# Kernel tuning notes

Hardware: AMD Instinct MI355X
Metric: run time of the kernel (lower is better)

## Reference

```python
import jax, jax.numpy as jnp
import numpy as np

NUM_HEADS = 12


def setup_inputs() -> dict:
    key = jax.random.key(0)
    k0, k1, k2 = jax.random.split(key, 3)
    B, N, C = 32, 864, 768  # N = 2*t_h*t_w + s_h*s_w = 288 + 576
    x = jax.random.normal(k0, (B, N, C), dtype=jnp.float32)
    W_qkv = jax.random.normal(k1, (C, 3 * C), dtype=jnp.float32) * 0.02
    W_proj = jax.random.normal(k2, (C, C), dtype=jnp.float32) * 0.02
    b_proj = jnp.zeros((C,), dtype=jnp.float32)
    return {"x": x, "W_qkv": W_qkv, "W_proj": W_proj, "b_proj": b_proj,
            "t_h": 12, "t_w": 12, "s_h": 24, "s_w": 24}


def reference(x, W_qkv, W_proj, b_proj, t_h, t_w, s_h, s_w):
    B, N, C = x.shape
    H = NUM_HEADS
    d = C // H
    scale = d ** -0.5
    # qkv projection (no bias), shape [3, B, H, N, d]
    qkv = (x @ W_qkv).reshape(B, N, 3, H, d).transpose(2, 0, 3, 1, 4)
    q, k, v = qkv[0], qkv[1], qkv[2]
    Tt = 2 * t_h * t_w            # temporal (template) query tokens = 288
    Ts = s_h * s_w                # spatial (search) query tokens = 576
    Mt = 2 * ((t_h + 1) // 2) ** 2  # sub-sampled temporal kv tokens = 72
    Ms = (s_h * s_w) // 4           # sub-sampled spatial kv tokens = 144
    q_t, q_s = q[:, :, :Tt], q[:, :, Tt:Tt + Ts]
    k_t, k_s = k[:, :, :Mt], k[:, :, Mt:Mt + Ms]
    v_t, v_s = v[:, :, :Mt], v[:, :, Mt:Mt + Ms]
    # temporal queries attend spatial keys/values
    a_t = jax.nn.softmax(jnp.einsum('bhqd,bhkd->bhqk', q_t, k_s) * scale, axis=-1)
    x_t = jnp.einsum('bhqk,bhkd->bhqd', a_t, v_s).transpose(0, 2, 1, 3).reshape(B, Tt, C)
    # spatial queries attend temporal keys/values
    a_s = jax.nn.softmax(jnp.einsum('bhqd,bhkd->bhqk', q_s, k_t) * scale, axis=-1)
    x_s = jnp.einsum('bhqk,bhkd->bhqd', a_s, v_t).transpose(0, 2, 1, 3).reshape(B, Ts, C)
    out = jnp.concatenate([x_t, x_s], axis=1)  # [B, N, C]
    return out @ W_proj + b_proj
```

## Files before the change

### kernel.cpp

```cpp
#include <hip/hip_runtime.h>
#include <hip/hip_bf16.h>

typedef __attribute__((ext_vector_type(8))) short short8;
typedef __attribute__((ext_vector_type(4))) float floatx4;

#define MFMA16(a, b, c) __builtin_amdgcn_mfma_f32_16x16x32_bf16((a), (b), (c), 0, 0, 0)

static constexpr int Bb = 32, Nn = 864, Cc = 768, Hh = 12;
static constexpr int Mm = Bb * Nn;
static constexpr int NQKV = 3 * Cc;

__device__ __forceinline__ void gload_lds16(const __hip_bfloat16* g, __hip_bfloat16* l) {
    __builtin_amdgcn_global_load_lds((const __attribute__((address_space(1))) void*)g,
                                     (__attribute__((address_space(3))) void*)l, 16, 0, 0);
}

static constexpr int CVT_BLKS = (Mm * Cc / 4) / 256;
static constexpr int TQKV_BLKS = (NQKV / 32) * (Cc / 32);
static constexpr int TPROJ_BLKS = (Cc / 32) * (Cc / 32);

__global__ __launch_bounds__(256) void prep_kernel(const float* __restrict__ x,
                                                   const float* __restrict__ Wqkv,
                                                   const float* __restrict__ Wproj,
                                                   __hip_bfloat16* __restrict__ xb,
                                                   __hip_bfloat16* __restrict__ WqkvT,
                                                   __hip_bfloat16* __restrict__ WprojT) {
    __shared__ float tile[32][33];
    const int bx = blockIdx.x;
    if (bx < CVT_BLKS) {
        const int i = bx * 256 + threadIdx.x;
        const float4 v = ((const float4*)x)[i];
        __hip_bfloat16 o[4] = {__float2bfloat16(v.x), __float2bfloat16(v.y),
                               __float2bfloat16(v.z), __float2bfloat16(v.w)};
        ((uint2*)xb)[i] = *(const uint2*)o;
        return;
    }
    const float* in;
    __hip_bfloat16* out;
    int R, C, bid;
    if (bx < CVT_BLKS + TQKV_BLKS) {
        bid = bx - CVT_BLKS; in = Wqkv; out = WqkvT; R = Cc; C = NQKV;
    } else {
        bid = bx - CVT_BLKS - TQKV_BLKS; in = Wproj; out = WprojT; R = Cc; C = Cc;
    }
    const int c0 = (bid % (C / 32)) * 32, r0 = (bid / (C / 32)) * 32;
    const int tx = threadIdx.x & 31, ty = threadIdx.x >> 5;
#pragma unroll
    for (int i = 0; i < 32; i += 8)
        tile[ty + i][tx] = in[(size_t)(r0 + ty + i) * C + c0 + tx];
    __syncthreads();
#pragma unroll
    for (int i = 0; i < 32; i += 8)
        out[(size_t)(c0 + ty + i) * R + r0 + tx] = __float2bfloat16(tile[tx][ty + i]);
}

template <typename OutT>
__global__ __launch_bounds__(256) void gemm_bt(const __hip_bfloat16* __restrict__ A,
                                               const __hip_bfloat16* __restrict__ BT,
                                               OutT* __restrict__ Cout,
                                               const float* __restrict__ bias,
                                               int K, int Nout) {
    __shared__ __align__(16) __hip_bfloat16 As[8192];
    __shared__ __align__(16) __hip_bfloat16 Bs[8192];
    const int n0 = blockIdx.x * 128, m0 = blockIdx.y * 128;
    const int t = threadIdx.x;
    const int lane = t & 63, wave = t >> 6;
    const int wm = (wave >> 1) * 64, wn = (wave & 1) * 64;
    const int ln = lane & 15, quad = lane >> 4;

    floatx4 acc[4][4] = {};

    const int r0 = t >> 2;
    const int cst = (t & 3) * 8;
    const __hip_bfloat16* Ag = A + (size_t)(m0 + r0) * K + cst;
    const __hip_bfloat16* Bg = BT + (size_t)(n0 + r0) * K + cst;
    const size_t rowskip = (size_t)64 * K;

    for (int k0 = 0; k0 < K; k0 += 64) {
        gload_lds16(Ag + k0,                &As[t * 8]);
        gload_lds16(Ag + k0 + rowskip,      &As[2048 + t * 8]);
        gload_lds16(Ag + k0 + 32,           &As[4096 + t * 8]);
        gload_lds16(Ag + k0 + 32 + rowskip, &As[6144 + t * 8]);
        gload_lds16(Bg + k0,                &Bs[t * 8]);
        gload_lds16(Bg + k0 + rowskip,      &Bs[2048 + t * 8]);
        gload_lds16(Bg + k0 + 32,           &Bs[4096 + t * 8]);
        gload_lds16(Bg + k0 + 32 + rowskip, &Bs[6144 + t * 8]);
        __syncthreads();

#pragma unroll
        for (int s = 0; s < 2; s++) {
            short8 af[4], bfr[4];
#pragma unroll
            for (int i = 0; i < 4; i++)
                af[i] = *(const short8*)&As[s * 4096 + (wm + i * 16 + ln) * 32 + quad * 8];
#pragma unroll
            for (int j = 0; j < 4; j++)
                bfr[j] = *(const short8*)&Bs[s * 4096 + (wn + j * 16 + ln) * 32 + quad * 8];
#pragma unroll
            for (int i = 0; i < 4; i++)
#pragma unroll
                for (int j = 0; j < 4; j++)
                    acc[i][j] = MFMA16(af[i], bfr[j], acc[i][j]);
        }
        __syncthreads();
    }

#pragma unroll
    for (int j = 0; j < 4; j++) {
        const int n = n0 + wn + j * 16 + ln;
        const float bv = bias ? bias[n] : 0.0f;
#pragma unroll
        for (int i = 0; i < 4; i++) {
            const int mrow = m0 + wm + i * 16 + quad * 4;
#pragma unroll
            for (int r = 0; r < 4; r++) {
                const float val = acc[i][j][r] + bv;
                if constexpr (__is_same(OutT, float))
                    Cout[(size_t)(mrow + r) * Nout + n] = val;
                else
                    Cout[(size_t)(mrow + r) * Nout + n] = __float2bfloat16(val);
            }
        }
    }
}

template <int L, int QOFF, int KVOFF, int NQT, int NCH>
__device__ __forceinline__ void attn_part(const __hip_bfloat16* __restrict__ qkv,
                                          __hip_bfloat16* __restrict__ attn,
                                          int qc, int h, int b,
                                          __hip_bfloat16* Ks, __hip_bfloat16* VTs) {
    constexpr int RSTG = ((L + 15) / 16) * 16;
    constexpr int KPAD = NCH * 32;
    constexpr int VSTR = KPAD + 8;
    const int t = threadIdx.x, lane = t & 63, wave = t >> 6;
    const int ln = lane & 15, quad = lane >> 4;
    const __hip_bfloat16 z16 = __float2bfloat16(0.0f);

    const __hip_bfloat16* kbase = qkv + ((size_t)(b * 864 + KVOFF)) * 2304 + 768 + h * 64;
    const __hip_bfloat16* vbase = kbase + 768;

    for (int c = t; c < RSTG * 8; c += 256) {
        const int key = c >> 3, d0 = (c & 7) * 8;
        uint4 val = make_uint4(0u, 0u, 0u, 0u);
        if (key < L) val = *(const uint4*)(kbase + (size_t)key * 2304 + d0);
        *(uint4*)&Ks[key * 72 + d0] = val;
    }
    for (int c = t; c < KPAD * 8; c += 256) {
        const int key = c >> 3, d0 = (c & 7) * 8;
        if (key < L) {
            uint4 raw = *(const uint4*)(vbase + (size_t)key * 2304 + d0);
            const __hip_bfloat16* pv = (const __hip_bfloat16*)&raw;
#pragma unroll
            for (int jj = 0; jj < 8; jj++) VTs[(d0 + jj) * VSTR + key] = pv[jj];
        } else {
#pragma unroll
            for (int jj = 0; jj < 8; jj++) VTs[(d0 + jj) * VSTR + key] = z16;
        }
    }
    __syncthreads();

    const int qt = qc * 4 + wave;
    if (qt >= NQT) return;

    const __hip_bfloat16* qrow = qkv + (size_t)(b * 864 + QOFF + qt * 16 + ln) * 2304 + h * 64;
    const short8 aq0 = *(const short8*)(qrow + quad * 8);
    const short8 aq1 = *(const short8*)(qrow + 32 + quad * 8);

    float dsum = 0.0f;
    floatx4 acco[4] = {};
    constexpr float CSC = 0.18033688011112042f;

#pragma unroll
    for (int ch = 0; ch < NCH; ch++) {
        unsigned int pk[2][2];
#pragma unroll
        for (int ti2 = 0; ti2 < 2; ti2++) {
            const int ti = ch * 2 + ti2;
            if (ti * 16 >= L) {
                pk[ti2][0] = 0u; pk[ti2][1] = 0u;
                continue;
            }
            const __hip_bfloat16* krow = &Ks[(ti * 16 + ln) * 72];
            const short8 k0 = *(const short8*)(krow + quad * 8);
            const short8 k1 = *(const short8*)(krow + 32 + quad * 8);
            floatx4 s = {0.f, 0.f, 0.f, 0.f};
            s = MFMA16(k0, aq0, s);
            s = MFMA16(k1, aq1, s);
            float p[4];
#pragma unroll
            for (int r = 0; r < 4; r++) {
                float e = exp2f(s[r] * CSC);
                if (ti * 16 + 16 > L)
                    if (ti * 16 + quad * 4 + r >= L) e = 0.0f;
                p[r] = e;
                dsum += e;
            }
            const __hip_bfloat162 lo = __float22bfloat162_rn(make_float2(p[0], p[1]));
            const __hip_bfloat162 hi = __float22bfloat162_rn(make_float2(p[2], p[3]));
            pk[ti2][0] = *(const unsigned int*)&lo;
            pk[ti2][1] = *(const unsigned int*)&hi;
        }
        const int srcA = ln + ((quad & 1) << 5);
        const int srcB = srcA + 16;
        const unsigned int c0 = (unsigned int)__shfl((int)pk[0][0], srcA);
        const unsigned int c1 = (unsigned int)__shfl((int)pk[0][1], srcA);
        const unsigned int c2 = (unsigned int)__shfl((int)pk[0][0], srcB);
        const unsigned int c3 = (unsigned int)__shfl((int)pk[0][1], srcB);
        const unsigned int d0 = (unsigned int)__shfl((int)pk[1][0], srcA);
        const unsigned int d1 = (unsigned int)__shfl((int)pk[1][1], srcA);
        const unsigned int d2 = (unsigned int)__shfl((int)pk[1][0], srcB);
        const unsigned int d3 = (unsigned int)__shfl((int)pk[1][1], srcB);
        const bool hi2 = quad >= 2;
        union { unsigned int u[4]; short8 v; } pf;
        pf.u[0] = hi2 ? d0 : c0;
        pf.u[1] = hi2 ? d1 : c1;
        pf.u[2] = hi2 ? d2 : c2;
        pf.u[3] = hi2 ? d3 : c3;
#pragma unroll
        for (int j = 0; j < 4; j++) {
            const short8 vt = *(const short8*)&VTs[(j * 16 + ln) * VSTR + ch * 32 + quad * 8];
            acco[j] = MFMA16(vt, pf.v, acco[j]);
        }
    }

    dsum += __shfl_xor(dsum, 16);
    dsum += __shfl_xor(dsum, 32);
    const float inv = 1.0f / dsum;

    const size_t orow = (size_t)(b * 864 + QOFF + qt * 16 + ln) * 768 + h * 64;
#pragma unroll
    for (int j = 0; j < 4; j++) {
        const __hip_bfloat162 lo =
            __float22bfloat162_rn(make_float2(acco[j][0] * inv, acco[j][1] * inv));
        const __hip_bfloat162 hi =
            __float22bfloat162_rn(make_float2(acco[j][2] * inv, acco[j][3] * inv));
        uint2 o = make_uint2(*(const unsigned int*)&lo, *(const unsigned int*)&hi);
        *(uint2*)&attn[orow + j * 16 + quad * 4] = o;
    }
}

__global__ __launch_bounds__(256) void attn_fused(const __hip_bfloat16* __restrict__ qkv,
                                                  __hip_bfloat16* __restrict__ attn) {
    __shared__ __align__(16) __hip_bfloat16 Ks[144 * 72];
    __shared__ __align__(16) __hip_bfloat16 VTs[64 * 168];
    const int h = blockIdx.y, b = blockIdx.z;
    if (blockIdx.x < 5)
        attn_part<144, 0, 72, 18, 5>(qkv, attn, blockIdx.x, h, b, Ks, VTs);
    else
        attn_part<72, 288, 0, 36, 3>(qkv, attn, blockIdx.x - 5, h, b, Ks, VTs);
}

extern "C" void kernel_launch(void* const* d_in, const int* in_sizes, int n_in,
                              void* d_out, int out_size, void* d_ws, size_t ws_size,
                              hipStream_t stream) {
    const float* x     = (const float*)d_in[0];
    const float* Wqkv  = (const float*)d_in[1];
    const float* Wproj = (const float*)d_in[2];
    const float* bproj = (const float*)d_in[3];
    float* out = (float*)d_out;

    char* ws = (char*)d_ws;
    __hip_bfloat16* xb     = (__hip_bfloat16*)ws;
    __hip_bfloat16* WqkvT  = (__hip_bfloat16*)(ws + 42467328);
    __hip_bfloat16* WprojT = (__hip_bfloat16*)(ws + 46006272);
    __hip_bfloat16* qkv    = (__hip_bfloat16*)(ws + 47185920);
    __hip_bfloat16* attn   = (__hip_bfloat16*)ws;

    prep_kernel<<<CVT_BLKS + TQKV_BLKS + TPROJ_BLKS, 256, 0, stream>>>(x, Wqkv, Wproj, xb,
                                                                       WqkvT, WprojT);
    gemm_bt<__hip_bfloat16><<<dim3(NQKV / 128, Mm / 128), 256, 0, stream>>>(xb, WqkvT, qkv,
                                                                            nullptr, Cc, NQKV);
    attn_fused<<<dim3(14, Hh, Bb), 256, 0, stream>>>(qkv, attn);
    gemm_bt<float><<<dim3(Cc / 128, Mm / 128), 256, 0, stream>>>(attn, WprojT, out, bproj, Cc, Cc);
}
```

Before: 409.9 us.

## Compute K/V projections only for the sub-sampled rows and swizzle GEMM blocks

The QKV GEMM is split into a Q projection over all tokens and a K/V projection that covers only the first 256 rows per batch, since attention reads K/V only from rows 0..215. This removes roughly two thirds of the K/V projection FLOPs and writes. A block-index swizzle is also added to the GEMM that regroups workgroups in strides of 8, likely targeting XCD/cache locality. The cost is an extra kernel launch and separate Q and KV buffers.

```diff
diff --git a/kernel.cpp b/kernel.cpp
--- a/kernel.cpp
+++ b/kernel.cpp
@@ -9,6 +9,8 @@
 static constexpr int Bb = 32, Nn = 864, Cc = 768, Hh = 12;
 static constexpr int Mm = Bb * Nn;
 static constexpr int NQKV = 3 * Cc;
+static constexpr int NKV = 2 * Cc;
+static constexpr int KVROWS = 256;
 
 __device__ __forceinline__ void gload_lds16(const __hip_bfloat16* g, __hip_bfloat16* l) {
     __builtin_amdgcn_global_load_lds((const __attribute__((address_space(1))) void*)g,
@@ -54,7 +56,7 @@
         out[(size_t)(c0 + ty + i) * R + r0 + tx] = __float2bfloat16(tile[tx][ty + i]);
 }
 
-template <typename OutT>
+template <typename OutT, bool KVMODE>
 __global__ __launch_bounds__(256) void gemm_bt(const __hip_bfloat16* __restrict__ A,
                                                const __hip_bfloat16* __restrict__ BT,
                                                OutT* __restrict__ Cout,
@@ -62,7 +64,22 @@
                                                int K, int Nout) {
     __shared__ __align__(16) __hip_bfloat16 As[8192];
     __shared__ __align__(16) __hip_bfloat16 Bs[8192];
-    const int n0 = blockIdx.x * 128, m0 = blockIdx.y * 128;
+    const int gx = (int)gridDim.x;
+    const int nwg = gx * (int)gridDim.y;
+    const int braw = (int)blockIdx.y * gx + (int)blockIdx.x;
+    const int cpx = nwg >> 3;
+    const int sid = (braw & 7) * cpx + (braw >> 3);
+    const int mt = sid / gx, nt = sid - mt * gx;
+    int arow0, orow0;
+    if constexpr (KVMODE) {
+        const int b = mt >> 1, r = (mt & 1) << 7;
+        arow0 = b * Nn + r;
+        orow0 = b * KVROWS + r;
+    } else {
+        arow0 = mt << 7;
+        orow0 = arow0;
+    }
+    const int n0 = nt * 128;
     const int t = threadIdx.x;
     const int lane = t & 63, wave = t >> 6;
     const int wm = (wave >> 1) * 64, wn = (wave & 1) * 64;
@@ -72,7 +89,7 @@
 
     const int r0 = t >> 2;
     const int cst = (t & 3) * 8;
-    const __hip_bfloat16* Ag = A + (size_t)(m0 + r0) * K + cst;
+    const __hip_bfloat16* Ag = A + (size_t)(arow0 + r0) * K + cst;
     const __hip_bfloat16* Bg = BT + (size_t)(n0 + r0) * K + cst;
     const size_t rowskip = (size_t)64 * K;
 
@@ -111,7 +128,7 @@
         const float bv = bias ? bias[n] : 0.0f;
 #pragma unroll
         for (int i = 0; i < 4; i++) {
-            const int mrow = m0 + wm + i * 16 + quad * 4;
+            const int mrow = orow0 + wm + i * 16 + quad * 4;
 #pragma unroll
             for (int r = 0; r < 4; r++) {
                 const float val = acc[i][j][r] + bv;
@@ -125,7 +142,8 @@
 }
 
 template <int L, int QOFF, int KVOFF, int NQT, int NCH>
-__device__ __forceinline__ void attn_part(const __hip_bfloat16* __restrict__ qkv,
+__device__ __forceinline__ void attn_part(const __hip_bfloat16* __restrict__ qb,
+                                          const __hip_bfloat16* __restrict__ kv,
                                           __hip_bfloat16* __restrict__ attn,
                                           int qc, int h, int b,
                                           __hip_bfloat16* Ks, __hip_bfloat16* VTs) {
@@ -136,19 +154,19 @@
     const int ln = lane & 15, quad = lane >> 4;
     const __hip_bfloat16 z16 = __float2bfloat16(0.0f);
 
-    const __hip_bfloat16* kbase = qkv + ((size_t)(b * 864 + KVOFF)) * 2304 + 768 + h * 64;
-    const __hip_bfloat16* vbase = kbase + 768;
+    const __hip_bfloat16* kbase = kv + (size_t)(b * KVROWS + KVOFF) * NKV + h * 64;
+    const __hip_bfloat16* vbase = kbase + Cc;
 
     for (int c = t; c < RSTG * 8; c += 256) {
         const int key = c >> 3, d0 = (c & 7) * 8;
         uint4 val = make_uint4(0u, 0u, 0u, 0u);
-        if (key < L) val = *(const uint4*)(kbase + (size_t)key * 2304 + d0);
+        if (key < L) val = *(const uint4*)(kbase + (size_t)key * NKV + d0);
         *(uint4*)&Ks[key * 72 + d0] = val;
     }
     for (int c = t; c < KPAD * 8; c += 256) {
         const int key = c >> 3, d0 = (c & 7) * 8;
         if (key < L) {
-            uint4 raw = *(const uint4*)(vbase + (size_t)key * 2304 + d0);
+            uint4 raw = *(const uint4*)(vbase + (size_t)key * NKV + d0);
             const __hip_bfloat16* pv = (const __hip_bfloat16*)&raw;
 #pragma unroll
             for (int jj = 0; jj < 8; jj++) VTs[(d0 + jj) * VSTR + key] = pv[jj];
@@ -162,7 +180,7 @@
     const int qt = qc * 4 + wave;
     if (qt >= NQT) return;
 
-    const __hip_bfloat16* qrow = qkv + (size_t)(b * 864 + QOFF + qt * 16 + ln) * 2304 + h * 64;
+    const __hip_bfloat16* qrow = qb + (size_t)(b * Nn + QOFF + qt * 16 + ln) * Cc + h * 64;
     const short8 aq0 = *(const short8*)(qrow + quad * 8);
     const short8 aq1 = *(const short8*)(qrow + 32 + quad * 8);
 
@@ -227,7 +245,7 @@
     dsum += __shfl_xor(dsum, 32);
     const float inv = 1.0f / dsum;
 
-    const size_t orow = (size_t)(b * 864 + QOFF + qt * 16 + ln) * 768 + h * 64;
+    const size_t orow = (size_t)(b * Nn + QOFF + qt * 16 + ln) * 768 + h * 64;
 #pragma unroll
     for (int j = 0; j < 4; j++) {
         const __hip_bfloat162 lo =
@@ -239,15 +257,16 @@
     }
 }
 
-__global__ __launch_bounds__(256) void attn_fused(const __hip_bfloat16* __restrict__ qkv,
+__global__ __launch_bounds__(256) void attn_fused(const __hip_bfloat16* __restrict__ qb,
+                                                  const __hip_bfloat16* __restrict__ kv,
                                                   __hip_bfloat16* __restrict__ attn) {
     __shared__ __align__(16) __hip_bfloat16 Ks[144 * 72];
     __shared__ __align__(16) __hip_bfloat16 VTs[64 * 168];
     const int h = blockIdx.y, b = blockIdx.z;
     if (blockIdx.x < 5)
-        attn_part<144, 0, 72, 18, 5>(qkv, attn, blockIdx.x, h, b, Ks, VTs);
+        attn_part<144, 0, 72, 18, 5>(qb, kv, attn, blockIdx.x, h, b, Ks, VTs);
     else
-        attn_part<72, 288, 0, 36, 3>(qkv, attn, blockIdx.x - 5, h, b, Ks, VTs);
+        attn_part<72, 288, 0, 36, 3>(qb, kv, attn, blockIdx.x - 5, h, b, Ks, VTs);
 }
 
 extern "C" void kernel_launch(void* const* d_in, const int* in_sizes, int n_in,
@@ -263,13 +282,17 @@
     __hip_bfloat16* xb     = (__hip_bfloat16*)ws;
     __hip_bfloat16* WqkvT  = (__hip_bfloat16*)(ws + 42467328);
     __hip_bfloat16* WprojT = (__hip_bfloat16*)(ws + 46006272);
-    __hip_bfloat16* qkv    = (__hip_bfloat16*)(ws + 47185920);
+    __hip_bfloat16* Qbuf   = (__hip_bfloat16*)(ws + 47185920);
+    __hip_bfloat16* KVbuf  = (__hip_bfloat16*)(ws + 89653248);
     __hip_bfloat16* attn   = (__hip_bfloat16*)ws;
 
     prep_kernel<<<CVT_BLKS + TQKV_BLKS + TPROJ_BLKS, 256, 0, stream>>>(x, Wqkv, Wproj, xb,
                                                                        WqkvT, WprojT);
-    gemm_bt<__hip_bfloat16><<<dim3(NQKV / 128, Mm / 128), 256, 0, stream>>>(xb, WqkvT, qkv,
-                                                                            nullptr, Cc, NQKV);
-    attn_fused<<<dim3(14, Hh, Bb), 256, 0, stream>>>(qkv, attn);
-    gemm_bt<float><<<dim3(Cc / 128, Mm / 128), 256, 0, stream>>>(attn, WprojT, out, bproj, Cc, Cc);
-}
+    gemm_bt<__hip_bfloat16, false><<<dim3(Cc / 128, Mm / 128), 256, 0, stream>>>(
+        xb, WqkvT, Qbuf, nullptr, Cc, Cc);
+    gemm_bt<__hip_bfloat16, true><<<dim3(NKV / 128, Bb * KVROWS / 128), 256, 0, stream>>>(
+        xb, WqkvT + (size_t)Cc * Cc, KVbuf, nullptr, Cc, NKV);
+    attn_fused<<<dim3(14, Hh, Bb), 256, 0, stream>>>(Qbuf, KVbuf, attn);
+    gemm_bt<float, false><<<dim3(Cc / 128, Mm / 128), 256, 0, stream>>>(attn, WprojT, out,
+                                                                        bproj, Cc, Cc);
+}
```

New measurement: 330.4 us. 1.24x faster.

## Compute only needed K/V rows in QKV GEMM, write V transposed, simplify attention

Applied to the files above, without the earlier changes.

Splits the QKV GEMM so Q is computed for all tokens but K and V only for the first 256 rows per batch (216 are used). V is transposed through LDS in the epilogue into a per-batch VT buffer. Attention drops LDS staging, reads K and VT directly from global memory, and processes two query tiles per wave. A workgroup index swizzle is added to both GEMMs. This cuts wasted projection FLOPs and the strided V transposition, at the cost of more global/L2 traffic in attention.

```diff
diff --git a/kernel.cpp b/kernel.cpp
--- a/kernel.cpp
+++ b/kernel.cpp
@@ -8,7 +8,7 @@
 
 static constexpr int Bb = 32, Nn = 864, Cc = 768, Hh = 12;
 static constexpr int Mm = Bb * Nn;
-static constexpr int NQKV = 3 * Cc;
+static constexpr int KVROWS = 256;
 
 __device__ __forceinline__ void gload_lds16(const __hip_bfloat16* g, __hip_bfloat16* l) {
     __builtin_amdgcn_global_load_lds((const __attribute__((address_space(1))) void*)g,
@@ -16,7 +16,7 @@
 }
 
 static constexpr int CVT_BLKS = (Mm * Cc / 4) / 256;
-static constexpr int TQKV_BLKS = (NQKV / 32) * (Cc / 32);
+static constexpr int TQKV_BLKS = (3 * Cc / 32) * (Cc / 32);
 static constexpr int TPROJ_BLKS = (Cc / 32) * (Cc / 32);
 
 __global__ __launch_bounds__(256) void prep_kernel(const float* __restrict__ x,
@@ -39,7 +39,7 @@
     __hip_bfloat16* out;
     int R, C, bid;
     if (bx < CVT_BLKS + TQKV_BLKS) {
-        bid = bx - CVT_BLKS; in = Wqkv; out = WqkvT; R = Cc; C = NQKV;
+        bid = bx - CVT_BLKS; in = Wqkv; out = WqkvT; R = Cc; C = 3 * Cc;
     } else {
         bid = bx - CVT_BLKS - TQKV_BLKS; in = Wproj; out = WprojT; R = Cc; C = Cc;
     }
@@ -54,15 +54,46 @@
         out[(size_t)(c0 + ty + i) * R + r0 + tx] = __float2bfloat16(tile[tx][ty + i]);
 }
 
-template <typename OutT>
-__global__ __launch_bounds__(256) void gemm_bt(const __hip_bfloat16* __restrict__ A,
-                                               const __hip_bfloat16* __restrict__ BT,
-                                               OutT* __restrict__ Cout,
-                                               const float* __restrict__ bias,
-                                               int K, int Nout) {
-    __shared__ __align__(16) __hip_bfloat16 As[8192];
-    __shared__ __align__(16) __hip_bfloat16 Bs[8192];
-    const int n0 = blockIdx.x * 128, m0 = blockIdx.y * 128;
+static constexpr int QBLKS = 6 * (Mm / 128);
+static constexpr int KVBLKS = 12 * (Bb * KVROWS / 128);
+static constexpr int QKV_NWG = QBLKS + KVBLKS;
+
+__global__ __launch_bounds__(256) void gemm_qkv(const __hip_bfloat16* __restrict__ A,
+                                                const __hip_bfloat16* __restrict__ WqkvT,
+                                                __hip_bfloat16* __restrict__ Qbuf,
+                                                __hip_bfloat16* __restrict__ Kbuf,
+                                                __hip_bfloat16* __restrict__ VTbuf) {
+    __shared__ __align__(16) char SMEM[34816];
+    __hip_bfloat16* As = (__hip_bfloat16*)SMEM;
+    __hip_bfloat16* Bs = As + 8192;
+
+    const int braw = (int)blockIdx.x;
+    const int sid = (braw & 7) * (QKV_NWG / 8) + (braw >> 3);
+
+    int arow0, orow0, btrow, ncol0, bb = 0, keybase = 0;
+    __hip_bfloat16* Out;
+    int Nout;
+    bool vmode = false;
+    if (sid < QBLKS) {
+        const int nt = sid % 6, mt = sid / 6;
+        arow0 = mt * 128; orow0 = arow0;
+        btrow = nt * 128; ncol0 = nt * 128;
+        Out = Qbuf; Nout = Cc;
+    } else {
+        const int s = sid - QBLKS;
+        const int nt = s % 12, mt = s / 12;
+        bb = mt >> 1; keybase = (mt & 1) << 7;
+        arow0 = bb * Nn + keybase;
+        btrow = Cc + nt * 128;
+        if (nt < 6) {
+            orow0 = bb * KVROWS + keybase; ncol0 = nt * 128;
+            Out = Kbuf; Nout = Cc;
+        } else {
+            vmode = true; ncol0 = (nt - 6) * 128;
+            Out = nullptr; Nout = 0; orow0 = 0;
+        }
+    }
+
     const int t = threadIdx.x;
     const int lane = t & 63, wave = t >> 6;
     const int wm = (wave >> 1) * 64, wn = (wave & 1) * 64;
@@ -72,11 +103,11 @@
 
     const int r0 = t >> 2;
     const int cst = (t & 3) * 8;
-    const __hip_bfloat16* Ag = A + (size_t)(m0 + r0) * K + cst;
-    const __hip_bfloat16* Bg = BT + (size_t)(n0 + r0) * K + cst;
-    const size_t rowskip = (size_t)64 * K;
-
-    for (int k0 = 0; k0 < K; k0 += 64) {
+    const __hip_bfloat16* Ag = A + (size_t)(arow0 + r0) * Cc + cst;
+    const __hip_bfloat16* Bg = WqkvT + (size_t)(btrow + r0) * Cc + cst;
+    const size_t rowskip = (size_t)64 * Cc;
+
+    for (int k0 = 0; k0 < Cc; k0 += 64) {
         gload_lds16(Ag + k0,                &As[t * 8]);
         gload_lds16(Ag + k0 + rowskip,      &As[2048 + t * 8]);
         gload_lds16(Ag + k0 + 32,           &As[4096 + t * 8]);
@@ -105,149 +136,254 @@
         __syncthreads();
     }
 
+    if (!vmode) {
+#pragma unroll
+        for (int j = 0; j < 4; j++) {
+            const int n = ncol0 + wn + j * 16 + ln;
+#pragma unroll
+            for (int i = 0; i < 4; i++) {
+                const int mrow = orow0 + wm + i * 16 + quad * 4;
+#pragma unroll
+                for (int r = 0; r < 4; r++)
+                    Out[(size_t)(mrow + r) * Nout + n] = __float2bfloat16(acc[i][j][r]);
+            }
+        }
+        return;
+    }
+
+    __hip_bfloat16* T = (__hip_bfloat16*)SMEM;
+#pragma unroll
+    for (int j = 0; j < 4; j++) {
+        const int ddl = wn + j * 16 + ln;
+#pragma unroll
+        for (int i = 0; i < 4; i++) {
+            const int key = wm + i * 16 + quad * 4;
+#pragma unroll
+            for (int r = 0; r < 4; r++)
+                T[ddl * 136 + key + r] = __float2bfloat16(acc[i][j][r]);
+        }
+    }
+    __syncthreads();
+#pragma unroll
+    for (int it = 0; it < 8; it++) {
+        const int ldd = it * 16 + (t >> 4);
+        const int kk = (t & 15) * 8;
+        const short8 v = *(const short8*)&T[ldd * 136 + kk];
+        *(short8*)&VTbuf[(size_t)(bb * Cc + ncol0 + ldd) * KVROWS + keybase + kk] = v;
+    }
+}
+
+__global__ __launch_bounds__(256) void gemm_proj(const __hip_bfloat16* __restrict__ A,
+                                                 const __hip_bfloat16* __restrict__ BT,
+                                                 float* __restrict__ Cout,
+                                                 const float* __restrict__ bias) {
+    __shared__ __align__(16) __hip_bfloat16 As[8192];
+    __shared__ __align__(16) __hip_bfloat16 Bs[8192];
+    const int gx = (int)gridDim.x;
+    const int nwg = gx * (int)gridDim.y;
+    const int braw = (int)blockIdx.y * gx + (int)blockIdx.x;
+    const int sid = (braw & 7) * (nwg >> 3) + (braw >> 3);
+    const int mt = sid / gx, nt = sid - mt * gx;
+    const int m0 = mt << 7, n0 = nt * 128;
+    const int t = threadIdx.x;
+    const int lane = t & 63, wave = t >> 6;
+    const int wm = (wave >> 1) * 64, wn = (wave & 1) * 64;
+    const int ln = lane & 15, quad = lane >> 4;
+
+    floatx4 acc[4][4] = {};
+    const int r0 = t >> 2, cst = (t & 3) * 8;
+    const __hip_bfloat16* Ag = A + (size_t)(m0 + r0) * Cc + cst;
+    const __hip_bfloat16* Bg = BT + (size_t)(n0 + r0) * Cc + cst;
+    const size_t rowskip = (size_t)64 * Cc;
+
+    for (int k0 = 0; k0 < Cc; k0 += 64) {
+        gload_lds16(Ag + k0,                &As[t * 8]);
+        gload_lds16(Ag + k0 + rowskip,      &As[2048 + t * 8]);
+        gload_lds16(Ag + k0 + 32,           &As[4096 + t * 8]);
+        gload_lds16(Ag + k0 + 32 + rowskip, &As[6144 + t * 8]);
+        gload_lds16(Bg + k0,                &Bs[t * 8]);
+        gload_lds16(Bg + k0 + rowskip,      &Bs[2048 + t * 8]);
+        gload_lds16(Bg + k0 + 32,           &Bs[4096 + t * 8]);
+        gload_lds16(Bg + k0 + 32 + rowskip, &Bs[6144 + t * 8]);
+        __syncthreads();
+#pragma unroll
+        for (int s = 0; s < 2; s++) {
+            short8 af[4], bfr[4];
+#pragma unroll
+            for (int i = 0; i < 4; i++)
+                af[i] = *(const short8*)&As[s * 4096 + (wm + i * 16 + ln) * 32 + quad * 8];
+#pragma unroll
+            for (int j = 0; j < 4; j++)
+                bfr[j] = *(const short8*)&Bs[s * 4096 + (wn + j * 16 + ln) * 32 + quad * 8];
+#pragma unroll
+            for (int i = 0; i < 4; i++)
+#pragma unroll
+                for (int j = 0; j < 4; j++)
+                    acc[i][j] = MFMA16(af[i], bfr[j], acc[i][j]);
+        }
+        __syncthreads();
+    }
 #pragma unroll
     for (int j = 0; j < 4; j++) {
         const int n = n0 + wn + j * 16 + ln;
-        const float bv = bias ? bias[n] : 0.0f;
+        const float bv = bias[n];
 #pragma unroll
         for (int i = 0; i < 4; i++) {
             const int mrow = m0 + wm + i * 16 + quad * 4;
 #pragma unroll
-            for (int r = 0; r < 4; r++) {
-                const float val = acc[i][j][r] + bv;
-                if constexpr (__is_same(OutT, float))
-                    Cout[(size_t)(mrow + r) * Nout + n] = val;
-                else
-                    Cout[(size_t)(mrow + r) * Nout + n] = __float2bfloat16(val);
-            }
-        }
-    }
-}
-
-template <int L, int QOFF, int KVOFF, int NQT, int NCH>
-__device__ __forceinline__ void attn_part(const __hip_bfloat16* __restrict__ qkv,
+            for (int r = 0; r < 4; r++)
+                Cout[(size_t)(mrow + r) * Cc + n] = acc[i][j][r] + bv;
+        }
+    }
+}
+
+template <int L, int QOFF, int KVOFF, int NCH>
+__device__ __forceinline__ void attn_pair(const __hip_bfloat16* __restrict__ qb,
+                                          const __hip_bfloat16* __restrict__ kb,
+                                          const __hip_bfloat16* __restrict__ vtb,
                                           __hip_bfloat16* __restrict__ attn,
-                                          int qc, int h, int b,
-                                          __hip_bfloat16* Ks, __hip_bfloat16* VTs) {
-    constexpr int RSTG = ((L + 15) / 16) * 16;
-    constexpr int KPAD = NCH * 32;
-    constexpr int VSTR = KPAD + 8;
-    const int t = threadIdx.x, lane = t & 63, wave = t >> 6;
+                                          int p, int h, int b) {
+    const int lane = threadIdx.x & 63;
     const int ln = lane & 15, quad = lane >> 4;
-    const __hip_bfloat16 z16 = __float2bfloat16(0.0f);
-
-    const __hip_bfloat16* kbase = qkv + ((size_t)(b * 864 + KVOFF)) * 2304 + 768 + h * 64;
-    const __hip_bfloat16* vbase = kbase + 768;
-
-    for (int c = t; c < RSTG * 8; c += 256) {
-        const int key = c >> 3, d0 = (c & 7) * 8;
-        uint4 val = make_uint4(0u, 0u, 0u, 0u);
-        if (key < L) val = *(const uint4*)(kbase + (size_t)key * 2304 + d0);
-        *(uint4*)&Ks[key * 72 + d0] = val;
-    }
-    for (int c = t; c < KPAD * 8; c += 256) {
-        const int key = c >> 3, d0 = (c & 7) * 8;
-        if (key < L) {
-            uint4 raw = *(const uint4*)(vbase + (size_t)key * 2304 + d0);
-            const __hip_bfloat16* pv = (const __hip_bfloat16*)&raw;
-#pragma unroll
-            for (int jj = 0; jj < 8; jj++) VTs[(d0 + jj) * VSTR + key] = pv[jj];
-        } else {
-#pragma unroll
-            for (int jj = 0; jj < 8; jj++) VTs[(d0 + jj) * VSTR + key] = z16;
-        }
-    }
-    __syncthreads();
-
-    const int qt = qc * 4 + wave;
-    if (qt >= NQT) return;
-
-    const __hip_bfloat16* qrow = qkv + (size_t)(b * 864 + QOFF + qt * 16 + ln) * 2304 + h * 64;
-    const short8 aq0 = *(const short8*)(qrow + quad * 8);
-    const short8 aq1 = *(const short8*)(qrow + 32 + quad * 8);
-
-    float dsum = 0.0f;
-    floatx4 acco[4] = {};
+
+    const __hip_bfloat16* kbase = kb + (size_t)(b * KVROWS + KVOFF) * Cc + h * 64;
+    const __hip_bfloat16* vtbase = vtb + (size_t)(b * Cc + h * 64) * KVROWS + KVOFF;
+
+    const int qt0 = 2 * p;
+    const __hip_bfloat16* qrowA =
+        qb + (size_t)(b * Nn + QOFF + qt0 * 16 + ln) * Cc + h * 64;
+    const __hip_bfloat16* qrowB = qrowA + (size_t)16 * Cc;
+    const short8 aqA0 = *(const short8*)(qrowA + quad * 8);
+    const short8 aqA1 = *(const short8*)(qrowA + 32 + quad * 8);
+    const short8 aqB0 = *(const short8*)(qrowB + quad * 8);
+    const short8 aqB1 = *(const short8*)(qrowB + 32 + quad * 8);
+
+    float dsA = 0.0f, dsB = 0.0f;
+    floatx4 accA[4] = {}, accB[4] = {};
     constexpr float CSC = 0.18033688011112042f;
 
 #pragma unroll
     for (int ch = 0; ch < NCH; ch++) {
-        unsigned int pk[2][2];
+        unsigned int pkA[2][2] = {}, pkB[2][2] = {};
 #pragma unroll
         for (int ti2 = 0; ti2 < 2; ti2++) {
             const int ti = ch * 2 + ti2;
-            if (ti * 16 >= L) {
-                pk[ti2][0] = 0u; pk[ti2][1] = 0u;
-                continue;
-            }
-            const __hip_bfloat16* krow = &Ks[(ti * 16 + ln) * 72];
+            if (ti * 16 >= L) continue;
+            const __hip_bfloat16* krow = kbase + (size_t)(ti * 16 + ln) * Cc;
             const short8 k0 = *(const short8*)(krow + quad * 8);
             const short8 k1 = *(const short8*)(krow + 32 + quad * 8);
-            floatx4 s = {0.f, 0.f, 0.f, 0.f};
-            s = MFMA16(k0, aq0, s);
-            s = MFMA16(k1, aq1, s);
-            float p[4];
+            floatx4 sA = {0.f, 0.f, 0.f, 0.f}, sB = {0.f, 0.f, 0.f, 0.f};
+            sA = MFMA16(k0, aqA0, sA);
+            sA = MFMA16(k1, aqA1, sA);
+            sB = MFMA16(k0, aqB0, sB);
+            sB = MFMA16(k1, aqB1, sB);
+            float pA[4], pB[4];
 #pragma unroll
             for (int r = 0; r < 4; r++) {
-                float e = exp2f(s[r] * CSC);
-                if (ti * 16 + 16 > L)
-                    if (ti * 16 + quad * 4 + r >= L) e = 0.0f;
-                p[r] = e;
-                dsum += e;
+                float eA = exp2f(sA[r] * CSC);
+                float eB = exp2f(sB[r] * CSC);
+                if (ti * 16 + 16 > L) {
+                    if (ti * 16 + quad * 4 + r >= L) { eA = 0.0f; eB = 0.0f; }
+                }
+                pA[r] = eA; dsA += eA;
+                pB[r] = eB; dsB += eB;
             }
-            const __hip_bfloat162 lo = __float22bfloat162_rn(make_float2(p[0], p[1]));
-            const __hip_bfloat162 hi = __float22bfloat162_rn(make_float2(p[2], p[3]));
-            pk[ti2][0] = *(const unsigned int*)&lo;
-            pk[ti2][1] = *(const unsigned int*)&hi;
+            {
+                const __hip_bfloat162 lo = __float22bfloat162_rn(make_float2(pA[0], pA[1]));
+                const __hip_bfloat162 hi = __float22bfloat162_rn(make_float2(pA[2], pA[3]));
+                pkA[ti2][0] = *(const unsigned int*)&lo;
+                pkA[ti2][1] = *(const unsigned int*)&hi;
+            }
+            {
+                const __hip_bfloat162 lo = __float22bfloat162_rn(make_float2(pB[0], pB[1]));
+                const __hip_bfloat162 hi = __float22bfloat162_rn(make_float2(pB[2], pB[3]));
+                pkB[ti2][0] = *(const unsigned int*)&lo;
+                pkB[ti2][1] = *(const unsigned int*)&hi;
+            }
         }
         const int srcA = ln + ((quad & 1) << 5);
         const int srcB = srcA + 16;
-        const unsigned int c0 = (unsigned int)__shfl((int)pk[0][0], srcA);
-        const unsigned int c1 = (unsigned int)__shfl((int)pk[0][1], srcA);
-        const unsigned int c2 = (unsigned int)__shfl((int)pk[0][0], srcB);
-        const unsigned int c3 = (unsigned int)__shfl((int)pk[0][1], srcB);
-        const unsigned int d0 = (unsigned int)__shfl((int)pk[1][0], srcA);
-        const unsigned int d1 = (unsigned int)__shfl((int)pk[1][1], srcA);
-        const unsigned int d2 = (unsigned int)__shfl((int)pk[1][0], srcB);
-        const unsigned int d3 = (unsigned int)__shfl((int)pk[1][1], srcB);
         const bool hi2 = quad >= 2;
-        union { unsigned int u[4]; short8 v; } pf;
-        pf.u[0] = hi2 ? d0 : c0;
-        pf.u[1] = hi2 ? d1 : c1;
-        pf.u[2] = hi2 ? d2 : c2;
-        pf.u[3] = hi2 ? d3 : c3;
+        union { unsigned int u[4]; short8 v; } pfA, pfB;
+        {
+            const unsigned int c0 = (unsigned int)__shfl((int)pkA[0][0], srcA);
+            const unsigned int c1 = (unsigned int)__shfl((int)pkA[0][1], srcA);
+            const unsigned int c2 = (unsigned int)__shfl((int)pkA[0][0], srcB);
+            const unsigned int c3 = (unsigned int)__shfl((int)pkA[0][1], srcB);
+            const unsigned int d0 = (unsigned int)__shfl((int)pkA[1][0], srcA);
+            const unsigned int d1 = (unsigned int)__shfl((int)pkA[1][1], srcA);
+            const unsigned int d2 = (unsigned int)__shfl((int)pkA[1][0], srcB);
+            const unsigned int d3 = (unsigned int)__shfl((int)pkA[1][1], srcB);
+            pfA.u[0] = hi2 ? d0 : c0;
+            pfA.u[1] = hi2 ? d1 : c1;
+            pfA.u[2] = hi2 ? d2 : c2;
+            pfA.u[3] = hi2 ? d3 : c3;
+        }
+        {
+            const unsigned int c0 = (unsigned int)__shfl((int)pkB[0][0], srcA);
+            const unsigned int c1 = (unsigned int)__shfl((int)pkB[0][1], srcA);
+            const unsigned int c2 = (unsigned int)__shfl((int)pkB[0][0], srcB);
+            const unsigned int c3 = (unsigned int)__shfl((int)pkB[0][1], srcB);
+            const unsigned int d0 = (unsigned int)__shfl((int)pkB[1][0], srcA);
+            const unsigned int d1 = (unsigned int)__shfl((int)pkB[1][1], srcA);
+            const unsigned int d2 = (unsigned int)__shfl((int)pkB[1][0], srcB);
+            const unsigned int d3 = (unsigned int)__shfl((int)pkB[1][1], srcB);
+            pfB.u[0] = hi2 ? d0 : c0;
+            pfB.u[1] = hi2 ? d1 : c1;
+            pfB.u[2] = hi2 ? d2 : c2;
+            pfB.u[3] = hi2 ? d3 : c3;
+        }
 #pragma unroll
         for (int j = 0; j < 4; j++) {
-            const short8 vt = *(const short8*)&VTs[(j * 16 + ln) * VSTR + ch * 32 + quad * 8];
-            acco[j] = MFMA16(vt, pf.v, acco[j]);
-        }
-    }
-
-    dsum += __shfl_xor(dsum, 16);
-    dsum += __shfl_xor(dsum, 32);
-    const float inv = 1.0f / dsum;
-
-    const size_t orow = (size_t)(b * 864 + QOFF + qt * 16 + ln) * 768 + h * 64;
+            const short8 vt =
+                *(const short8*)&vtbase[(size_t)(j * 16 + ln) * KVROWS + ch * 32 + quad * 8];
+            accA[j] = MFMA16(vt, pfA.v, accA[j]);
+            accB[j] = MFMA16(vt, pfB.v, accB[j]);
+        }
+    }
+
+    dsA += __shfl_xor(dsA, 16); dsA += __shfl_xor(dsA, 32);
+    dsB += __shfl_xor(dsB, 16); dsB += __shfl_xor(dsB, 32);
+    const float invA = 1.0f / dsA, invB = 1.0f / dsB;
+
+    const size_t orowA = (size_t)(b * Nn + QOFF + qt0 * 16 + ln) * Cc + h * 64;
+    const size_t orowB = orowA + (size_t)16 * Cc;
 #pragma unroll
     for (int j = 0; j < 4; j++) {
-        const __hip_bfloat162 lo =
-            __float22bfloat162_rn(make_float2(acco[j][0] * inv, acco[j][1] * inv));
-        const __hip_bfloat162 hi =
-            __float22bfloat162_rn(make_float2(acco[j][2] * inv, acco[j][3] * inv));
-        uint2 o = make_uint2(*(const unsigned int*)&lo, *(const unsigned int*)&hi);
-        *(uint2*)&attn[orow + j * 16 + quad * 4] = o;
-    }
-}
-
-__global__ __launch_bounds__(256) void attn_fused(const __hip_bfloat16* __restrict__ qkv,
+        {
+            const __hip_bfloat162 lo =
+                __float22bfloat162_rn(make_float2(accA[j][0] * invA, accA[j][1] * invA));
+            const __hip_bfloat162 hi =
+                __float22bfloat162_rn(make_float2(accA[j][2] * invA, accA[j][3] * invA));
+            uint2 o = make_uint2(*(const unsigned int*)&lo, *(const unsigned int*)&hi);
+            *(uint2*)&attn[orowA + j * 16 + quad * 4] = o;
+        }
+        {
+            const __hip_bfloat162 lo =
+                __float22bfloat162_rn(make_float2(accB[j][0] * invB, accB[j][1] * invB));
+            const __hip_bfloat162 hi =
+                __float22bfloat162_rn(make_float2(accB[j][2] * invB, accB[j][3] * invB));
+            uint2 o = make_uint2(*(const unsigned int*)&lo, *(const unsigned int*)&hi);
+            *(uint2*)&attn[orowB + j * 16 + quad * 4] = o;
+        }
+    }
+}
+
+static constexpr int ATTN_BLKS = (384 * 27) / 4;
+
+__global__ __launch_bounds__(256) void attn_fused(const __hip_bfloat16* __restrict__ qb,
+                                                  const __hip_bfloat16* __restrict__ kb,
+                                                  const __hip_bfloat16* __restrict__ vtb,
                                                   __hip_bfloat16* __restrict__ attn) {
-    __shared__ __align__(16) __hip_bfloat16 Ks[144 * 72];
-    __shared__ __align__(16) __hip_bfloat16 VTs[64 * 168];
-    const int h = blockIdx.y, b = blockIdx.z;
-    if (blockIdx.x < 5)
-        attn_part<144, 0, 72, 18, 5>(qkv, attn, blockIdx.x, h, b, Ks, VTs);
+    const int rid = (int)blockIdx.x;
+    const int vid = (rid & 7) * (ATTN_BLKS / 8) + (rid >> 3);
+    const int g = vid * 4 + (threadIdx.x >> 6);
+    const int bh = g / 27, slot = g - bh * 27;
+    const int h = bh % 12, b = bh / 12;
+    if (slot < 9)
+        attn_pair<144, 0, 72, 5>(qb, kb, vtb, attn, slot, h, b);
     else
-        attn_part<72, 288, 0, 36, 3>(qkv, attn, blockIdx.x - 5, h, b, Ks, VTs);
+        attn_pair<72, 288, 0, 3>(qb, kb, vtb, attn, slot - 9, h, b);
 }
 
 extern "C" void kernel_launch(void* const* d_in, const int* in_sizes, int n_in,
@@ -263,13 +399,14 @@
     __hip_bfloat16* xb     = (__hip_bfloat16*)ws;
     __hip_bfloat16* WqkvT  = (__hip_bfloat16*)(ws + 42467328);
     __hip_bfloat16* WprojT = (__hip_bfloat16*)(ws + 46006272);
-    __hip_bfloat16* qkv    = (__hip_bfloat16*)(ws + 47185920);
+    __hip_bfloat16* Qbuf   = (__hip_bfloat16*)(ws + 47185920);
+    __hip_bfloat16* Kbuf   = (__hip_bfloat16*)(ws + 89653248);
+    __hip_bfloat16* VTbuf  = (__hip_bfloat16*)(ws + 102236160);
     __hip_bfloat16* attn   = (__hip_bfloat16*)ws;
 
     prep_kernel<<<CVT_BLKS + TQKV_BLKS + TPROJ_BLKS, 256, 0, stream>>>(x, Wqkv, Wproj, xb,
                                                                        WqkvT, WprojT);
-    gemm_bt<__hip_bfloat16><<<dim3(NQKV / 128, Mm / 128), 256, 0, stream>>>(xb, WqkvT, qkv,
-                                                                            nullptr, Cc, NQKV);
-    attn_fused<<<dim3(14, Hh, Bb), 256, 0, stream>>>(qkv, attn);
-    gemm_bt<float><<<dim3(Cc / 128, Mm / 128), 256, 0, stream>>>(attn, WprojT, out, bproj, Cc, Cc);
-}
+    gemm_qkv<<<QKV_NWG, 256, 0, stream>>>(xb, WqkvT, Qbuf, Kbuf, VTbuf);
+    attn_fused<<<ATTN_BLKS, 256, 0, stream>>>(Qbuf, Kbuf, VTbuf, attn);
+    gemm_proj<<<dim3(Cc / 128, Mm / 128), 256, 0, stream>>>(attn, WprojT, out, bproj);
+}
```

Result: faster. 343.8 us (-16.1%).
